# Kernel optimization log

Hardware: AMD Instinct MI355X
Metric: run time of the kernel (lower is better)

Reference implementation:

```python
import jax, jax.numpy as jnp
from jax import lax
import numpy as np

K = 11          # NUM_TAGS
S = K + 2       # with start/stop
START, STOP = K, K + 1
O_TAG = 0
B, T = 4096, 1024
NEG = -10000.0


def setup_inputs() -> dict:
    key = jax.random.key(0)
    k1, k2, k3 = jax.random.split(key, 3)
    e = jax.random.normal(k1, (B, T, K), dtype=jnp.float32)
    Tmat = jax.random.normal(k2, (S, S), dtype=jnp.float32) * 0.1
    Tmat = Tmat.at[:, START].set(NEG)
    Tmat = Tmat.at[STOP, :].set(NEG)
    Tmat = Tmat.at[O_TAG, O_TAG].add(-2.0)
    tags = jax.random.randint(k3, (B, T), 0, K, dtype=jnp.int32)
    mask = jnp.ones((B, T), dtype=bool)
    return {"e": e, "Tmat": Tmat, "tags": tags, "mask": mask}


def _nll(e, Tmat, tags, mask):
    maskf = mask.astype(e.dtype)
    # ---- forward algorithm (log partition) via scan over time ----
    a0 = jnp.full((e.shape[0], S), NEG, dtype=e.dtype).at[:, START].set(0.0)

    def step(a, inp):
        e_t, m_t = inp                                   # (B,K), (B,)
        # scores[b, to] = lse_from(a[b, from] + Tmat[from, to])
        sc = jax.nn.logsumexp(a[:, :, None] + Tmat[None, :, :], axis=1)  # (B,S)
        sc = sc.at[:, :K].add(e_t)
        a = jnp.where(m_t[:, None], sc, a)
        return a, None

    a, _ = lax.scan(step, a0, (jnp.swapaxes(e, 0, 1), jnp.swapaxes(mask, 0, 1)))
    logZ = jax.nn.logsumexp(a[:, :K] + Tmat[:K, STOP][None, :], axis=1)  # (B,)

    # ---- gold path score (fully vectorized) ----
    tg = jnp.clip(tags, 0, K - 1)
    em = jnp.take_along_axis(e, tg[:, :, None], axis=2)[..., 0] * maskf  # (B,T)
    trans = Tmat[tg[:, :-1], tg[:, 1:]] * maskf[:, 1:]                   # (B,T-1)
    last = mask.astype(jnp.int32).sum(1) - 1                             # (B,)
    last_tag = jnp.take_along_axis(tg, last[:, None], axis=1)[:, 0]
    gold = Tmat[START, tg[:, 0]] + em.sum(1) + trans.sum(1) + Tmat[last_tag, STOP]

    return jnp.mean(logZ - gold)


def reference(e, Tmat, tags, mask):
    return _nll(e, Tmat, tags, mask)
```

## Files before the change

### kernel.cpp

```cpp
#include <hip/hip_runtime.h>

#define KTAGS 11
#define SS    13
#define TT    1024
#define BB    4096
#define GPW   4
#define UNR   16
#define HALF  512

#define WS_VA   0
#define WS_UB   (11*BB)
#define WS_CF   (22*BB)
#define WS_EF   (23*BB)
#define WS_CB   (24*BB)
#define WS_EB   (25*BB)
#define WS_NLL  (26*BB)
#define WS_FLOATS (27*BB)

#define ROTSUM(A0,A1,A2,A3,SRC)                                                \
        asm volatile(                                                          \
          "s_nop 1\n\t"                                                        \
          "v_mul_f32 %0, %4, %5\n\t"                                           \
          "v_mul_f32_dpp %1, %4, %6  row_ror:1  row_mask:0xf bank_mask:0xf\n\t"\
          "v_mul_f32_dpp %2, %4, %7  row_ror:2  row_mask:0xf bank_mask:0xf\n\t"\
          "v_mul_f32_dpp %3, %4, %8  row_ror:3  row_mask:0xf bank_mask:0xf\n\t"\
          "v_fmac_f32_dpp %0, %4, %9  row_ror:4  row_mask:0xf bank_mask:0xf\n\t"\
          "v_fmac_f32_dpp %1, %4, %10 row_ror:5  row_mask:0xf bank_mask:0xf\n\t"\
          "v_fmac_f32_dpp %2, %4, %11 row_ror:6  row_mask:0xf bank_mask:0xf\n\t"\
          "v_fmac_f32_dpp %3, %4, %12 row_ror:7  row_mask:0xf bank_mask:0xf\n\t"\
          "v_fmac_f32_dpp %0, %4, %13 row_ror:8  row_mask:0xf bank_mask:0xf\n\t"\
          "v_fmac_f32_dpp %1, %4, %14 row_ror:9  row_mask:0xf bank_mask:0xf\n\t"\
          "v_fmac_f32_dpp %2, %4, %15 row_ror:10 row_mask:0xf bank_mask:0xf\n\t"\
          "v_fmac_f32_dpp %3, %4, %16 row_ror:11 row_mask:0xf bank_mask:0xf\n\t"\
          "v_fmac_f32_dpp %0, %4, %17 row_ror:12 row_mask:0xf bank_mask:0xf\n\t"\
          "v_fmac_f32_dpp %1, %4, %18 row_ror:13 row_mask:0xf bank_mask:0xf\n\t"\
          "v_fmac_f32_dpp %2, %4, %19 row_ror:14 row_mask:0xf bank_mask:0xf\n\t"\
          "v_fmac_f32_dpp %3, %4, %20 row_ror:15 row_mask:0xf bank_mask:0xf\n\t"\
          : "=&v"(A0), "=&v"(A1), "=&v"(A2), "=&v"(A3)                         \
          : "v"(SRC), "v"(W[0]), "v"(W[1]), "v"(W[2]),  "v"(W[3]),             \
            "v"(W[4]), "v"(W[5]), "v"(W[6]),  "v"(W[7]), "v"(W[8]),            \
            "v"(W[9]), "v"(W[10]), "v"(W[11]), "v"(W[12]), "v"(W[13]),         \
            "v"(W[14]), "v"(W[15]))

#define MAXRED(MM, SRC)                                                        \
        asm volatile(                                                          \
          "s_nop 1\n\t"                                                        \
          "v_max_f32_dpp %0, %1, %1 row_ror:8 row_mask:0xf bank_mask:0xf\n\t"  \
          "s_nop 1\n\t"                                                        \
          "v_max_f32_dpp %0, %0, %0 row_ror:4 row_mask:0xf bank_mask:0xf\n\t"  \
          "s_nop 1\n\t"                                                        \
          "v_max_f32_dpp %0, %0, %0 quad_perm:[1,0,3,2] row_mask:0xf bank_mask:0xf\n\t"\
          "s_nop 1\n\t"                                                        \
          "v_max_f32_dpp %0, %0, %0 quad_perm:[2,3,0,1] row_mask:0xf bank_mask:0xf\n\t"\
          : "=&v"(MM) : "v"(SRC))

#define STEP(J, E_T, TG)                                                       \
    {                                                                          \
        const float X_T = __expf(E_T);                                         \
        float ac0, ac1, ac2, ac3;                                              \
        ROTSUM(ac0, ac1, ac2, ac3, aP);                                        \
        float xsc = X_T;                                                       \
        if (((J) & 7) == 0) { cacc += eeP * 0.6931471805599453f; xsc *= scP; } \
        aP = ((ac0 + ac1) + (ac2 + ac3)) * xsc;                                \
        if (((J) & 7) == 7) {                                                  \
            float mm;                                                          \
            MAXRED(mm, aP);                                                    \
            const int ee = (int)((__float_as_uint(mm) >> 23) & 0xFFu) - 127;   \
            scP = __uint_as_float((unsigned)(127 - ee) << 23);                 \
            eeP = (float)ee;                                                   \
        }                                                                      \
        em_acc += (to == (TG)) ? (E_T) : 0.f;                                  \
    }

template<int DIR>
__device__ __forceinline__ void scan_dir(const float* __restrict__ e,
                                         const int*   __restrict__ tags,
                                         const float* sT,
                                         float*       __restrict__ ws,
                                         int b, int to)
{
    const int toT = (to < SS) ? to : (SS - 1);
    const int toE = (to < KTAGS) ? to : (KTAGS - 1);

    float W[16];
#pragma unroll
    for (int r = 0; r < 16; ++r) {
        const int f = (to - r) & 15;
        if (DIR > 0) {
            W[r] = (f < KTAGS && to <= SS - 1 && to != KTAGS)
                     ? __expf(sT[f * SS + toT]) : 0.f;
            if (to >= SS) W[r] = 0.f;
        } else {
            W[r] = (to < KTAGS && f < KTAGS) ? __expf(sT[to * SS + f]) : 0.f;
        }
    }

    const float* ebase = e    + (size_t)b * TT * KTAGS + toE;
    const int*   tbase = tags + (size_t)b * TT;

    float aP, em_acc, cacc = 0.f;
    if (DIR > 0) {
        const float E0 = ebase[0];
        const int   tg0 = tbase[0];
        aP = (to < SS) ? __expf(sT[(SS - 2) * SS + toT] + E0) : 0.f;
        em_acc = (to == tg0) ? E0 : 0.f;
    } else {
        const float E0 = ebase[(size_t)(TT - 1) * KTAGS];
        const int   tg0 = tbase[TT - 1];
        aP = (to < KTAGS) ? __expf(E0 + sT[toT * SS + (SS - 1)]) : 0.f;
        em_acc = (to == tg0) ? E0 : 0.f;
    }

    const ptrdiff_t estep = (ptrdiff_t)DIR * KTAGS;
    const float* peU = ebase + ((DIR > 0) ? (ptrdiff_t)KTAGS : (ptrdiff_t)(TT - 2) * KTAGS);
    const int*   tgU = tbase + ((DIR > 0) ? 1 : (TT - 2));

    float ebuf[UNR]; int tbuf[UNR];
#pragma unroll
    for (int j = 0; j < UNR; ++j) {
        ebuf[j] = peU[estep * j];
        tbuf[j] = tgU[DIR * j];
    }

    float scP = 1.f, eeP = 0.f;
    const float* qe = peU + estep * UNR;
    const int*   qt = tgU + DIR * UNR;

    for (int tb = 0; tb + 2 * UNR <= (HALF - 1); tb += UNR) {
#pragma unroll
        for (int j = 0; j < UNR; ++j) {
            const float E_T = ebuf[j];
            const int   TG  = tbuf[j];
            ebuf[j] = qe[estep * j];
            tbuf[j] = qt[DIR * j];
            STEP(j, E_T, TG)
        }
        qe += estep * UNR; qt += DIR * UNR;
    }
#pragma unroll
    for (int j = 0; j < UNR; ++j) {
        const float E_T = ebuf[j];
        const int   TG  = tbuf[j];
        if (j < UNR - 1) { ebuf[j] = qe[estep * j]; tbuf[j] = qt[DIR * j]; }
        STEP(j, E_T, TG)
    }
#pragma unroll
    for (int j = 0; j < UNR - 1; ++j) {
        STEP(j, ebuf[j], tbuf[j])
    }

    float em = em_acc;
#pragma unroll
    for (int s = 8; s >= 1; s >>= 1) em += __shfl_xor(em, s, 16);

    if (DIR > 0) {
        float ac0, ac1, ac2, ac3;
        ROTSUM(ac0, ac1, ac2, ac3, aP);
        const float v = (ac0 + ac1) + (ac2 + ac3);
        if (to < KTAGS) ws[WS_VA + to * BB + b] = v;
        if (to == 0) { ws[WS_CF + b] = cacc; ws[WS_EF + b] = em; }
    } else {
        if (to < KTAGS) ws[WS_UB + to * BB + b] = aP;
        if (to == 0) { ws[WS_CB + b] = cacc; ws[WS_EB + b] = em; }
    }
}

__global__ __launch_bounds__(64, 2)
void crf_scan2_kernel(const float* __restrict__ e,
                      const float* __restrict__ Tmat,
                      const int*   __restrict__ tags,
                      float*       __restrict__ ws)
{
    __shared__ float sT[SS * SS];
    const int tid = threadIdx.x;
    for (int i = tid; i < SS * SS; i += 64) sT[i] = Tmat[i];
    __syncthreads();

    const int g  = tid >> 4;
    const int to = tid & 15;
    const int b  = ((int)blockIdx.x & (BB / GPW - 1)) * GPW + g;

    if ((int)blockIdx.x < BB / GPW) scan_dir<+1>(e, tags, sT, ws, b, to);
    else                            scan_dir<-1>(e, tags, sT, ws, b, to);
}

__global__ __launch_bounds__(256)
void combine_kernel(float* __restrict__ ws)
{
    const int b = blockIdx.x * 256 + threadIdx.x;
    double dot = 0.0;
#pragma unroll
    for (int s = 0; s < KTAGS; ++s)
        dot += (double)ws[WS_VA + s * BB + b] * (double)ws[WS_UB + s * BB + b];
    const float logZ = (float)((double)ws[WS_CF + b] + (double)ws[WS_CB + b] + log(dot));
    ws[WS_NLL + b] = logZ - ws[WS_EF + b] - ws[WS_EB + b];
}

__global__ __launch_bounds__(64)
void gold_kernel(const float* __restrict__ Tmat,
                 const int*   __restrict__ tags,
                 float*       __restrict__ nll)
{
    __shared__ float sT[SS * SS];
    __shared__ int   stg[TT];
    const int tid = threadIdx.x;
    const int b   = blockIdx.x;

    for (int i = tid; i < SS * SS; i += 64) sT[i] = Tmat[i];
    const int4* tg4 = (const int4*)(tags + (size_t)b * TT);
    int4* s4 = (int4*)stg;
#pragma unroll
    for (int k = 0; k < TT / 4 / 64; ++k) s4[tid + 64 * k] = tg4[tid + 64 * k];
    __syncthreads();

    float s = 0.f;
    const int t0 = tid * 16;
#pragma unroll
    for (int k = 1; k <= 16; ++k) {
        const int t = t0 + k;
        if (t < TT) s += sT[stg[t - 1] * SS + stg[t]];
    }
    if (tid == 0) {
        s += sT[(SS - 2) * SS + stg[0]];
        s += sT[stg[TT - 1] * SS + (SS - 1)];
    }
#pragma unroll
    for (int d = 32; d >= 1; d >>= 1) s += __shfl_xor(s, d, 64);
    if (tid == 0) nll[b] -= s;
}

__global__ __launch_bounds__(256)
void reduce_mean_kernel(const float* __restrict__ v, float* __restrict__ out, int n)
{
    __shared__ double sbuf[256];
    double s = 0.0;
    for (int i = threadIdx.x; i < n; i += 256) s += (double)v[i];
    sbuf[threadIdx.x] = s;
    __syncthreads();
    for (int k = 128; k > 0; k >>= 1) {
        if ((int)threadIdx.x < k) sbuf[threadIdx.x] += sbuf[threadIdx.x + k];
        __syncthreads();
    }
    if (threadIdx.x == 0) out[0] = (float)(sbuf[0] / (double)n);
}

__global__ __launch_bounds__(64, 2)
void crf_scan_full_kernel(const float* __restrict__ e,
                          const float* __restrict__ Tmat,
                          const int*   __restrict__ tags,
                          float*       __restrict__ out_per_b)
{
    __shared__ float sT[SS * SS];
    const int tid = threadIdx.x;
    for (int i = tid; i < SS * SS; i += 64) sT[i] = Tmat[i];

    const int g   = tid >> 4;
    const int to  = tid & 15;
    const int toT = (to < SS) ? to : (SS - 1);
    const int toE = (to < KTAGS) ? to : (KTAGS - 1);
    const int b   = blockIdx.x * GPW + g;
    __syncthreads();

    float W[16];
#pragma unroll
    for (int r = 0; r < 16; ++r) {
        const int f = (to - r) & 15;
        W[r] = (f < KTAGS && to <= SS - 1 && to != KTAGS)
                 ? __expf(sT[f * SS + toT]) : 0.f;
        if (to >= SS) W[r] = 0.f;
    }
    const float eTstop = __expf(sT[toT * SS + (SS - 1)]);

    const float* pe  = e    + (size_t)b * TT * KTAGS + toE;
    const int*   tgp = tags + (size_t)b * TT;

    const float e0  = pe[0];
    const int   tg0 = tgp[0];
    float aP = (to < SS) ? __expf(sT[(SS - 2) * SS + toT] + e0) : 0.f;
    float cacc = 0.f;
    float em_acc = (to == tg0) ? e0 : 0.f;

    float ebuf[UNR]; int tbuf[UNR];
#pragma unroll
    for (int j = 0; j < UNR; ++j) {
        ebuf[j] = pe[(size_t)(1 + j) * KTAGS];
        tbuf[j] = tgp[1 + j];
    }
    float scP = 1.f, eeP = 0.f;

    const float* qe = pe  + (size_t)(1 + UNR) * KTAGS;
    const int*   qt = tgp + 1 + UNR;
    for (int tb = 1; tb + 2 * UNR <= TT; tb += UNR) {
#pragma unroll
        for (int j = 0; j < UNR; ++j) {
            const float E_T = ebuf[j];
            const int   TG  = tbuf[j];
            ebuf[j] = qe[j * KTAGS];
            tbuf[j] = qt[j];
            STEP(j, E_T, TG)
        }
        qe += (size_t)UNR * KTAGS; qt += UNR;
    }
#pragma unroll
    for (int j = 0; j < UNR; ++j) {
        const float E_T = ebuf[j];
        const int   TG  = tbuf[j];
        if (j < UNR - 1) { ebuf[j] = qe[j * KTAGS]; tbuf[j] = qt[j]; }
        STEP(j, E_T, TG)
    }
#pragma unroll
    for (int j = 0; j < UNR - 1; ++j) {
        STEP(j, ebuf[j], tbuf[j])
    }

    float z  = (to < KTAGS) ? aP * eTstop : 0.f;
    float em = em_acc;
#pragma unroll
    for (int s = 8; s >= 1; s >>= 1) {
        z  += __shfl_xor(z,  s, 16);
        em += __shfl_xor(em, s, 16);
    }
    if (to == 0) {
        const float logZ = cacc + __logf(z);
        out_per_b[b] = logZ - em;
    }
}

extern "C" void kernel_launch(void* const* d_in, const int* in_sizes, int n_in,
                              void* d_out, int out_size, void* d_ws, size_t ws_size,
                              hipStream_t stream)
{
    const float* e    = (const float*)d_in[0];
    const float* Tmat = (const float*)d_in[1];
    const int*   tags = (const int*)d_in[2];

    float* ws  = (float*)d_ws;
    float* out = (float*)d_out;

    if (ws_size >= (size_t)WS_FLOATS * sizeof(float)) {
        crf_scan2_kernel<<<2 * BB / GPW, 64, 0, stream>>>(e, Tmat, tags, ws);
        combine_kernel<<<BB / 256, 256, 0, stream>>>(ws);
        gold_kernel<<<BB, 64, 0, stream>>>(Tmat, tags, ws + WS_NLL);
        reduce_mean_kernel<<<1, 256, 0, stream>>>(ws + WS_NLL, out, BB);
    } else {
        crf_scan_full_kernel<<<BB / GPW, 64, 0, stream>>>(e, Tmat, tags, ws);
        gold_kernel<<<BB, 64, 0, stream>>>(Tmat, tags, ws);
        reduce_mean_kernel<<<1, 256, 0, stream>>>(ws, out, BB);
    }
}
```

Before: 80.59 us.

## Fuse gold-path transition sum into bidirectional scan and halve prefetch unroll

The transition-score part of the gold path is now computed inside each direction of the scan kernel, and the separate gold_kernel launch on the main path is dropped. This removes one kernel launch and a second pass over the tags array. The prefetch depth of the time loop is also cut from 16 to 8, which lowers register pressure but hides less global-load latency. The full-scan fallback drops its occupancy hint in launch_bounds.

```diff
diff --git a/kernel.cpp b/kernel.cpp
--- a/kernel.cpp
+++ b/kernel.cpp
@@ -6,7 +6,9 @@
 #define BB    4096
 #define GPW   4
 #define UNR   16
+#define PUNR  8
 #define HALF  512
+#define LN2   0.6931471805599453f
 
 #define WS_VA   0
 #define WS_UB   (11*BB)
@@ -60,7 +62,7 @@
         float ac0, ac1, ac2, ac3;                                              \
         ROTSUM(ac0, ac1, ac2, ac3, aP);                                        \
         float xsc = X_T;                                                       \
-        if (((J) & 7) == 0) { cacc += eeP * 0.6931471805599453f; xsc *= scP; } \
+        if (((J) & 7) == 0) { cacc += eeP * LN2; xsc *= scP; }                 \
         aP = ((ac0 + ac1) + (ac2 + ac3)) * xsc;                                \
         if (((J) & 7) == 7) {                                                  \
             float mm;                                                          \
@@ -115,38 +117,58 @@
     const float* peU = ebase + ((DIR > 0) ? (ptrdiff_t)KTAGS : (ptrdiff_t)(TT - 2) * KTAGS);
     const int*   tgU = tbase + ((DIR > 0) ? 1 : (TT - 2));
 
-    float ebuf[UNR]; int tbuf[UNR];
-#pragma unroll
-    for (int j = 0; j < UNR; ++j) {
+    float ebuf[PUNR]; int tbuf[PUNR];
+#pragma unroll
+    for (int j = 0; j < PUNR; ++j) {
         ebuf[j] = peU[estep * j];
         tbuf[j] = tgU[DIR * j];
     }
 
     float scP = 1.f, eeP = 0.f;
-    const float* qe = peU + estep * UNR;
-    const int*   qt = tgU + DIR * UNR;
-
-    for (int tb = 0; tb + 2 * UNR <= (HALF - 1); tb += UNR) {
-#pragma unroll
-        for (int j = 0; j < UNR; ++j) {
+    const float* qe = peU + estep * PUNR;
+    const int*   qt = tgU + DIR * PUNR;
+
+    for (int tb = 0; tb + 2 * PUNR <= (HALF - 1); tb += PUNR) {
+#pragma unroll
+        for (int j = 0; j < PUNR; ++j) {
             const float E_T = ebuf[j];
             const int   TG  = tbuf[j];
             ebuf[j] = qe[estep * j];
             tbuf[j] = qt[DIR * j];
             STEP(j, E_T, TG)
         }
-        qe += estep * UNR; qt += DIR * UNR;
-    }
-#pragma unroll
-    for (int j = 0; j < UNR; ++j) {
+        qe += estep * PUNR; qt += DIR * PUNR;
+    }
+#pragma unroll
+    for (int j = 0; j < PUNR; ++j) {
         const float E_T = ebuf[j];
         const int   TG  = tbuf[j];
-        if (j < UNR - 1) { ebuf[j] = qe[estep * j]; tbuf[j] = qt[DIR * j]; }
+        if (j < PUNR - 1) { ebuf[j] = qe[estep * j]; tbuf[j] = qt[DIR * j]; }
         STEP(j, E_T, TG)
     }
 #pragma unroll
-    for (int j = 0; j < UNR - 1; ++j) {
+    for (int j = 0; j < PUNR - 1; ++j) {
         STEP(j, ebuf[j], tbuf[j])
+    }
+
+    {
+        float tr = 0.f;
+        const int t0   = (DIR > 0) ? 1 : HALF;
+        const int tlim = (DIR > 0) ? (HALF - 1) : (TT - 1);
+#pragma unroll 4
+        for (int k = 0; k < 32; ++k) {
+            const int t = t0 + to + 16 * k;
+            if (t <= tlim) {
+                const int ta = tbase[t - 1];
+                const int tc = tbase[t];
+                tr += sT[ta * SS + tc];
+            }
+        }
+        if (to == 0) {
+            if (DIR > 0) tr += sT[(SS - 2) * SS + tbase[0]];
+            else         tr += sT[tbase[TT - 1] * SS + (SS - 1)];
+        }
+        em_acc += tr;
     }
 
     float em = em_acc;
@@ -196,39 +218,6 @@
     ws[WS_NLL + b] = logZ - ws[WS_EF + b] - ws[WS_EB + b];
 }
 
-__global__ __launch_bounds__(64)
-void gold_kernel(const float* __restrict__ Tmat,
-                 const int*   __restrict__ tags,
-                 float*       __restrict__ nll)
-{
-    __shared__ float sT[SS * SS];
-    __shared__ int   stg[TT];
-    const int tid = threadIdx.x;
-    const int b   = blockIdx.x;
-
-    for (int i = tid; i < SS * SS; i += 64) sT[i] = Tmat[i];
-    const int4* tg4 = (const int4*)(tags + (size_t)b * TT);
-    int4* s4 = (int4*)stg;
-#pragma unroll
-    for (int k = 0; k < TT / 4 / 64; ++k) s4[tid + 64 * k] = tg4[tid + 64 * k];
-    __syncthreads();
-
-    float s = 0.f;
-    const int t0 = tid * 16;
-#pragma unroll
-    for (int k = 1; k <= 16; ++k) {
-        const int t = t0 + k;
-        if (t < TT) s += sT[stg[t - 1] * SS + stg[t]];
-    }
-    if (tid == 0) {
-        s += sT[(SS - 2) * SS + stg[0]];
-        s += sT[stg[TT - 1] * SS + (SS - 1)];
-    }
-#pragma unroll
-    for (int d = 32; d >= 1; d >>= 1) s += __shfl_xor(s, d, 64);
-    if (tid == 0) nll[b] -= s;
-}
-
 __global__ __launch_bounds__(256)
 void reduce_mean_kernel(const float* __restrict__ v, float* __restrict__ out, int n)
 {
@@ -244,7 +233,40 @@
     if (threadIdx.x == 0) out[0] = (float)(sbuf[0] / (double)n);
 }
 
-__global__ __launch_bounds__(64, 2)
+__global__ __launch_bounds__(64)
+void gold_kernel(const float* __restrict__ Tmat,
+                 const int*   __restrict__ tags,
+                 float*       __restrict__ nll)
+{
+    __shared__ float sT[SS * SS];
+    __shared__ int   stg[TT];
+    const int tid = threadIdx.x;
+    const int b   = blockIdx.x;
+
+    for (int i = tid; i < SS * SS; i += 64) sT[i] = Tmat[i];
+    const int4* tg4 = (const int4*)(tags + (size_t)b * TT);
+    int4* s4 = (int4*)stg;
+#pragma unroll
+    for (int k = 0; k < TT / 4 / 64; ++k) s4[tid + 64 * k] = tg4[tid + 64 * k];
+    __syncthreads();
+
+    float s = 0.f;
+    const int t0 = tid * 16;
+#pragma unroll
+    for (int k = 1; k <= 16; ++k) {
+        const int t = t0 + k;
+        if (t < TT) s += sT[stg[t - 1] * SS + stg[t]];
+    }
+    if (tid == 0) {
+        s += sT[(SS - 2) * SS + stg[0]];
+        s += sT[stg[TT - 1] * SS + (SS - 1)];
+    }
+#pragma unroll
+    for (int d = 32; d >= 1; d >>= 1) s += __shfl_xor(s, d, 64);
+    if (tid == 0) nll[b] -= s;
+}
+
+__global__ __launch_bounds__(64)
 void crf_scan_full_kernel(const float* __restrict__ e,
                           const float* __restrict__ Tmat,
                           const int*   __restrict__ tags,
@@ -340,7 +362,6 @@
     if (ws_size >= (size_t)WS_FLOATS * sizeof(float)) {
         crf_scan2_kernel<<<2 * BB / GPW, 64, 0, stream>>>(e, Tmat, tags, ws);
         combine_kernel<<<BB / 256, 256, 0, stream>>>(ws);
-        gold_kernel<<<BB, 64, 0, stream>>>(Tmat, tags, ws + WS_NLL);
         reduce_mean_kernel<<<1, 256, 0, stream>>>(ws + WS_NLL, out, BB);
     } else {
         crf_scan_full_kernel<<<BB / GPW, 64, 0, stream>>>(e, Tmat, tags, ws);
```

New measurement: 78.89 us (median of 2 runs). 2.1% less time.
